# Kernel tuning notes

Measured on AMD Instinct MI355X. Metric: run time of the kernel, lower is better.

The kernel has to match this reference:

```python
import jax, jax.numpy as jnp
import numpy as np

S, T, B, V, E, H = 64, 48, 32, 32000, 512, 512


def setup_inputs() -> dict:
    key = jax.random.key(0)
    ks = jax.random.split(key, 24)
    def n(k, shape, s=0.05):
        return jax.random.normal(k, shape, dtype=jnp.float32) * s
    return {
        "src": jax.random.randint(ks[0], (S, B), 0, V),
        "trg": jax.random.randint(ks[1], (T, B), 0, V),
        "enc_emb": n(ks[2], (V, E)),
        "enc_Wih0": n(ks[3], (3 * H, E)),
        "enc_Whh0": n(ks[4], (3 * H, H)),
        "enc_bih0": n(ks[5], (3 * H,)),
        "enc_bhh0": n(ks[6], (3 * H,)),
        "enc_Wih1": n(ks[7], (3 * H, H)),
        "enc_Whh1": n(ks[8], (3 * H, H)),
        "enc_bih1": n(ks[9], (3 * H,)),
        "enc_bhh1": n(ks[10], (3 * H,)),
        "dec_emb": n(ks[11], (V, E)),
        "dec_Wih0": n(ks[12], (3 * H, E)),
        "dec_Whh0": n(ks[13], (3 * H, H)),
        "dec_bih0": n(ks[14], (3 * H,)),
        "dec_bhh0": n(ks[15], (3 * H,)),
        "dec_Wih1": n(ks[16], (3 * H, H)),
        "dec_Whh1": n(ks[17], (3 * H, H)),
        "dec_bih1": n(ks[18], (3 * H,)),
        "dec_bhh1": n(ks[19], (3 * H,)),
        "out_W": n(ks[20], (V, H)),
        "out_b": n(ks[21], (V,)),
    }


def gru_layer(xs, h0, Wih, Whh, bih, bhh):
    """PyTorch-convention GRU over a (T, B, D) sequence. Returns (ys, h_T)."""
    def step(h, x):
        gi = x @ Wih.T + bih          # (B, 3H)
        gh = h @ Whh.T + bhh          # (B, 3H)
        ir, iz, inn = jnp.split(gi, 3, axis=-1)
        hr, hz, hn = jnp.split(gh, 3, axis=-1)
        r = jax.nn.sigmoid(ir + hr)
        z = jax.nn.sigmoid(iz + hz)
        cand = jnp.tanh(inn + r * hn)
        h_new = (1.0 - z) * cand + z * h
        return h_new, h_new
    hT, ys = jax.lax.scan(step, h0, xs)
    return ys, hT


def reference(src, trg, enc_emb, enc_Wih0, enc_Whh0, enc_bih0, enc_bhh0,
              enc_Wih1, enc_Whh1, enc_bih1, enc_bhh1,
              dec_emb, dec_Wih0, dec_Whh0, dec_bih0, dec_bhh0,
              dec_Wih1, dec_Whh1, dec_bih1, dec_bhh1, out_W, out_b):
    b = src.shape[1]
    h = enc_Whh0.shape[1]
    h0 = jnp.zeros((b, h), dtype=enc_emb.dtype)
    # Encoder: 2-layer unidirectional GRU (dropout=0, eval mode)
    x = enc_emb[src]                                   # (S, B, E)
    y0, h0_f = gru_layer(x, h0, enc_Wih0, enc_Whh0, enc_bih0, enc_bhh0)
    _, h1_f = gru_layer(y0, h0, enc_Wih1, enc_Whh1, enc_bih1, enc_bhh1)
    # decoder_hidden = encoder_hidden[-2:] -> (layer0 final, layer1 final)
    # Decoder with teacher_forcing_ratio = 1.0: inputs are trg[:-1]
    d = dec_emb[trg[:-1]]                              # (T-1, B, E)
    d0, _ = gru_layer(d, h0_f, dec_Wih0, dec_Whh0, dec_bih0, dec_bhh0)
    d1, _ = gru_layer(d0, h1_f, dec_Wih1, dec_Whh1, dec_bih1, dec_bhh1)
    logits = d1 @ out_W.T + out_b                      # (T-1, B, V)
    return logits
```

## Files before the change

### kernel.cpp

```cpp
#include <hip/hip_runtime.h>
#include <hip/hip_bf16.h>

typedef __bf16 bf16x8 __attribute__((ext_vector_type(8)));
typedef float  f32x4  __attribute__((ext_vector_type(4)));

__device__ __forceinline__ void store_bf8(__bf16* dst, float4 a, float4 b) {
  bf16x8 v;
  v[0] = (__bf16)a.x; v[1] = (__bf16)a.y; v[2] = (__bf16)a.z; v[3] = (__bf16)a.w;
  v[4] = (__bf16)b.x; v[5] = (__bf16)b.y; v[6] = (__bf16)b.z; v[7] = (__bf16)b.w;
  *(bf16x8*)dst = v;
}

__device__ __forceinline__ bf16x8 load_coh16(const __bf16* p) {
  union { unsigned long long u[2]; bf16x8 v; } r;
  r.u[0] = __hip_atomic_load((const unsigned long long*)p,     __ATOMIC_RELAXED, __HIP_MEMORY_SCOPE_AGENT);
  r.u[1] = __hip_atomic_load((const unsigned long long*)p + 1, __ATOMIC_RELAXED, __HIP_MEMORY_SCOPE_AGENT);
  return r.v;
}

__device__ __forceinline__ void store_coh_bf16(__bf16* p, float v) {
  __bf16 b = (__bf16)v;
  unsigned short u;
  __builtin_memcpy(&u, &b, 2);
  __hip_atomic_store((unsigned short*)p, u, __ATOMIC_RELAXED, __HIP_MEMORY_SCOPE_AGENT);
}

__device__ __forceinline__ void wait_flags(const unsigned* f, unsigned tgt) {
  const unsigned* p = f + (threadIdx.x & 31) * 32;
  for (;;) {
    const unsigned v = __hip_atomic_load(p, __ATOMIC_RELAXED, __HIP_MEMORY_SCOPE_AGENT);
    if (__all((int)(v >= tgt))) break;
    __builtin_amdgcn_s_sleep(1);
  }
}

__global__ __launch_bounds__(256) void cvt_f32_bf16(
    const float* __restrict__ s, __bf16* __restrict__ d, long n8)
{
  long i = (long)blockIdx.x * 256 + threadIdx.x;
  if (i >= n8) return;
  const float4* sp = (const float4*)s + i * 2;
  store_bf8(d + i * 8, sp[0], sp[1]);
}

__global__ __launch_bounds__(64) void gather_cvt(
    const float* __restrict__ emb, const int* __restrict__ idx, __bf16* __restrict__ dst)
{
  const int r = blockIdx.x;
  const long row = idx[r];
  const float4* sp = (const float4*)(emb + row * 512) + threadIdx.x * 2;
  store_bf8(dst + (long)r * 512 + threadIdx.x * 8, sp[0], sp[1]);
}

__global__ __launch_bounds__(256) void gemm_bt(
    const __bf16* __restrict__ A, const __bf16* __restrict__ B,
    const float* __restrict__ bias, float* __restrict__ C, int M, int N)
{
  const int wave = threadIdx.x >> 6;
  const int lane = threadIdx.x & 63;
  const int l16 = lane & 15;
  const int quad = lane >> 4;

  const int m0 = blockIdx.x * 128 + wave * 32;
  const int n0 = blockIdx.y * 128;

  int r0 = m0 + l16;       if (r0 >= M) r0 = M - 1;
  int r1 = m0 + 16 + l16;  if (r1 >= M) r1 = M - 1;
  const __bf16* __restrict__ A0 = A + (long)r0 * 512 + quad * 8;
  const __bf16* __restrict__ A1 = A + (long)r1 * 512 + quad * 8;

  const __bf16* bp[8];
#pragma unroll
  for (int i = 0; i < 8; ++i)
    bp[i] = B + (long)(n0 + i * 16 + l16) * 512 + quad * 8;

  f32x4 acc[2][8];
#pragma unroll
  for (int mi = 0; mi < 2; ++mi)
#pragma unroll
    for (int i = 0; i < 8; ++i) acc[mi][i] = (f32x4){0.f, 0.f, 0.f, 0.f};

#pragma unroll
  for (int ks = 0; ks < 16; ++ks) {
    bf16x8 a0 = *(const bf16x8*)(A0 + ks * 32);
    bf16x8 a1 = *(const bf16x8*)(A1 + ks * 32);
#pragma unroll
    for (int i = 0; i < 8; ++i) {
      bf16x8 b = *(const bf16x8*)(bp[i] + ks * 32);
      acc[0][i] = __builtin_amdgcn_mfma_f32_16x16x32_bf16(a0, b, acc[0][i], 0, 0, 0);
      acc[1][i] = __builtin_amdgcn_mfma_f32_16x16x32_bf16(a1, b, acc[1][i], 0, 0, 0);
    }
  }

#pragma unroll
  for (int mi = 0; mi < 2; ++mi) {
    const int crow = m0 + mi * 16 + quad * 4;
#pragma unroll
    for (int i = 0; i < 8; ++i) {
      const int n = n0 + i * 16 + l16;
      const float bv = bias ? bias[n] : 0.0f;
#pragma unroll
      for (int r = 0; r < 4; ++r) {
        const int row = crow + r;
        if (row < M) C[(long)row * N + n] = acc[mi][i][r] + bv;
      }
    }
  }
}

__global__ __launch_bounds__(128) void gru2_pipe(
    const float* __restrict__ GI,
    const float* __restrict__ Whh0, const float* __restrict__ bhh0,
    const float* __restrict__ Wih1, const float* __restrict__ bih1,
    const float* __restrict__ Whh1, const float* __restrict__ bhh1,
    __bf16* __restrict__ Y0, __bf16* __restrict__ Y1,
    const __bf16* __restrict__ h0i, const __bf16* __restrict__ h1i,
    float* __restrict__ hf0, float* __restrict__ hf1,
    unsigned* __restrict__ flags0, unsigned* __restrict__ flags1, int T)
{
  __shared__ __align__(16) __bf16 wh[48 * 520];
  __shared__ __align__(16) __bf16 wi[48 * 520];

  const int tid = threadIdx.x;
  const int L   = blockIdx.x >> 5;
  const int c   = blockIdx.x & 31;
  const int w   = tid >> 6;
  const int lane = tid & 63;
  const int l16 = lane & 15;
  const int quad = lane >> 4;

  const float* __restrict__ Whh = L ? Whh1 : Whh0;
  const float* __restrict__ bhh = L ? bhh1 : bhh0;
  __bf16* __restrict__ Yown = L ? Y1 : Y0;
  const __bf16* __restrict__ hini = L ? h1i : h0i;
  float* __restrict__ hf = L ? hf1 : hf0;
  unsigned* __restrict__ fOwn = L ? flags1 : flags0;

  for (int ch = tid; ch < 48 * 64; ch += 128) {
    const int lr = ch >> 6, kc = ch & 63;
    const int g = lr >> 4, j = lr & 15;
    const float4* sp = (const float4*)(Whh + (long)(g * 512 + c * 16 + j) * 512) + kc * 2;
    store_bf8(&wh[lr * 520 + kc * 8], sp[0], sp[1]);
  }
  if (L) {
    for (int ch = tid; ch < 48 * 64; ch += 128) {
      const int lr = ch >> 6, kc = ch & 63;
      const int g = lr >> 4, j = lr & 15;
      const float4* sp = (const float4*)(Wih1 + (long)(g * 512 + c * 16 + j) * 512) + kc * 2;
      store_bf8(&wi[lr * 520 + kc * 8], sp[0], sp[1]);
    }
  }

  float bR = bhh[0 * 512 + c * 16 + l16];
  float bZ = bhh[1 * 512 + c * 16 + l16];
  float bH = bhh[2 * 512 + c * 16 + l16];
  float bN = 0.f;
  if (L) {
    bR += bih1[0 * 512 + c * 16 + l16];
    bZ += bih1[1 * 512 + c * 16 + l16];
    bN  = bih1[2 * 512 + c * 16 + l16];
  }
  __syncthreads();

  const int b0  = w * 16 + quad * 4;
  const int col = c * 16 + l16;

  float hprev[4];
#pragma unroll
  for (int r = 0; r < 4; ++r) hprev[r] = hf[(b0 + r) * 512 + col];

  for (int t = 0; t < T; ++t) {
    float giR[4] = {0, 0, 0, 0}, giZ[4] = {0, 0, 0, 0}, giN[4] = {0, 0, 0, 0};
    if (!L) {
      const float* GIt = GI + (long)t * 49152;
#pragma unroll
      for (int r = 0; r < 4; ++r) {
        const float* gp = GIt + (b0 + r) * 1536 + col;
        giR[r] = gp[0];
        giZ[r] = gp[512];
        giN[r] = gp[1024];
      }
    }

    if (L) {
      wait_flags(flags0, (unsigned)(t + 1));
      if (t) wait_flags(flags1, (unsigned)t);
    } else if (t) {
      wait_flags(flags0, (unsigned)t);
    }

    const __bf16* hsrc = t ? (Yown + (long)t * 16384) : hini;
    const __bf16* hA = hsrc + (w * 16 + l16) * 512 + quad * 8;
    bf16x8 ha[16], xa[16];
#pragma unroll
    for (int ks = 0; ks < 16; ++ks) ha[ks] = load_coh16(hA + ks * 32);
    if (L) {
      const __bf16* xA = Y0 + (long)(t + 1) * 16384 + (w * 16 + l16) * 512 + quad * 8;
#pragma unroll
      for (int ks = 0; ks < 16; ++ks) xa[ks] = load_coh16(xA + ks * 32);
    }

    f32x4 accR = {bR, bR, bR, bR};
    f32x4 accZ = {bZ, bZ, bZ, bZ};
    f32x4 accH = {bH, bH, bH, bH};
    f32x4 accN = {bN, bN, bN, bN};

#pragma unroll
    for (int ks = 0; ks < 16; ++ks) {
      const int o = ks * 32 + quad * 8;
      accR = __builtin_amdgcn_mfma_f32_16x16x32_bf16(ha[ks], *(const bf16x8*)&wh[(     l16) * 520 + o], accR, 0, 0, 0);
      accZ = __builtin_amdgcn_mfma_f32_16x16x32_bf16(ha[ks], *(const bf16x8*)&wh[(16 + l16) * 520 + o], accZ, 0, 0, 0);
      accH = __builtin_amdgcn_mfma_f32_16x16x32_bf16(ha[ks], *(const bf16x8*)&wh[(32 + l16) * 520 + o], accH, 0, 0, 0);
    }
    if (L) {
#pragma unroll
      for (int ks = 0; ks < 16; ++ks) {
        const int o = ks * 32 + quad * 8;
        accR = __builtin_amdgcn_mfma_f32_16x16x32_bf16(xa[ks], *(const bf16x8*)&wi[(     l16) * 520 + o], accR, 0, 0, 0);
        accZ = __builtin_amdgcn_mfma_f32_16x16x32_bf16(xa[ks], *(const bf16x8*)&wi[(16 + l16) * 520 + o], accZ, 0, 0, 0);
        accN = __builtin_amdgcn_mfma_f32_16x16x32_bf16(xa[ks], *(const bf16x8*)&wi[(32 + l16) * 520 + o], accN, 0, 0, 0);
      }
    }

    __bf16* yout = Yown + (long)(t + 1) * 16384;
#pragma unroll
    for (int r = 0; r < 4; ++r) {
      float rs = accR[r], zs = accZ[r], hn = accH[r], nn = accN[r];
      if (!L) { rs += giR[r]; zs += giZ[r]; nn = giN[r]; }
      const float rg = 1.0f / (1.0f + expf(-rs));
      const float zg = 1.0f / (1.0f + expf(-zs));
      const float cand = tanhf(nn + rg * hn);
      const float hnew = (1.0f - zg) * cand + zg * hprev[r];
      hprev[r] = hnew;
      store_coh_bf16(yout + (b0 + r) * 512 + col, hnew);
    }

    asm volatile("s_waitcnt vmcnt(0)" ::: "memory");
    __syncthreads();
    if (tid == 0)
      __hip_atomic_store(fOwn + c * 32, (unsigned)(t + 1),
                         __ATOMIC_RELAXED, __HIP_MEMORY_SCOPE_AGENT);
  }

#pragma unroll
  for (int r = 0; r < 4; ++r) hf[(b0 + r) * 512 + col] = hprev[r];
}

extern "C" void kernel_launch(void* const* d_in, const int* in_sizes, int n_in,
                              void* d_out, int out_size, void* d_ws, size_t ws_size,
                              hipStream_t stream)
{
  const int* src = (const int*)d_in[0];
  const int* trg = (const int*)d_in[1];
  const float* enc_emb  = (const float*)d_in[2];
  const float* enc_Wih0 = (const float*)d_in[3];
  const float* enc_Whh0 = (const float*)d_in[4];
  const float* enc_bih0 = (const float*)d_in[5];
  const float* enc_bhh0 = (const float*)d_in[6];
  const float* enc_Wih1 = (const float*)d_in[7];
  const float* enc_Whh1 = (const float*)d_in[8];
  const float* enc_bih1 = (const float*)d_in[9];
  const float* enc_bhh1 = (const float*)d_in[10];
  const float* dec_emb  = (const float*)d_in[11];
  const float* dec_Wih0 = (const float*)d_in[12];
  const float* dec_Whh0 = (const float*)d_in[13];
  const float* dec_bih0 = (const float*)d_in[14];
  const float* dec_bhh0 = (const float*)d_in[15];
  const float* dec_Wih1 = (const float*)d_in[16];
  const float* dec_Whh1 = (const float*)d_in[17];
  const float* dec_bih1 = (const float*)d_in[18];
  const float* dec_bhh1 = (const float*)d_in[19];
  const float* out_W    = (const float*)d_in[20];
  const float* out_b    = (const float*)d_in[21];

  char* ws = (char*)d_ws;
  float*  GI    = (float*)(ws + 0);
  __bf16* Xenc  = (__bf16*)(ws + 12582912);
  __bf16* Xdec  = (__bf16*)(ws + 14680064);
  __bf16* Y0e   = (__bf16*)(ws + 16220160);
  __bf16* Y1e   = (__bf16*)(ws + 18350080);
  __bf16* Y0d   = (__bf16*)(ws + 20480000);
  __bf16* Y1d   = (__bf16*)(ws + 22052864);
  __bf16* Wb0   = (__bf16*)(ws + 23625728);
  __bf16* Wb2   = (__bf16*)(ws + 25198592);
  __bf16* outWb = (__bf16*)(ws + 26771456);
  float*  hf0   = (float*)(ws + 59539456);
  float*  hf1   = (float*)(ws + 59604992);
  __bf16* zb    = (__bf16*)(ws + 59670528);
  unsigned* flags = (unsigned*)(ws + 59703296);

  hipMemsetAsync(hf0, 0, 131072, stream);
  hipMemsetAsync(zb, 0, 32768, stream);
  hipMemsetAsync(flags, 0, 16384, stream);

  gather_cvt<<<2048, 64, 0, stream>>>(enc_emb, src, Xenc);
  gather_cvt<<<1504, 64, 0, stream>>>(dec_emb, trg, Xdec);
  cvt_f32_bf16<<<384, 256, 0, stream>>>(enc_Wih0, Wb0, 98304);
  cvt_f32_bf16<<<384, 256, 0, stream>>>(dec_Wih0, Wb2, 98304);
  cvt_f32_bf16<<<8000, 256, 0, stream>>>(out_W, outWb, 2048000);

  gemm_bt<<<dim3(16, 12), 256, 0, stream>>>(Xenc, Wb0, enc_bih0, GI, 2048, 1536);
  gru2_pipe<<<64, 128, 0, stream>>>(GI, enc_Whh0, enc_bhh0,
                                    enc_Wih1, enc_bih1, enc_Whh1, enc_bhh1,
                                    Y0e, Y1e, zb, zb, hf0, hf1,
                                    flags + 0, flags + 1024, 64);
  gemm_bt<<<dim3(12, 12), 256, 0, stream>>>(Xdec, Wb2, dec_bih0, GI, 1504, 1536);
  gru2_pipe<<<64, 128, 0, stream>>>(GI, dec_Whh0, dec_bhh0,
                                    dec_Wih1, dec_bih1, dec_Whh1, dec_bhh1,
                                    Y0d, Y1d, Y0e + 64 * 16384, Y1e + 64 * 16384, hf0, hf1,
                                    flags + 2048, flags + 3072, 47);

  gemm_bt<<<dim3(12, 250), 256, 0, stream>>>(Y1d + 16384, outWb, out_b,
                                             (float*)d_out, 1504, 32000);
}
```

Measured before the change: 1.431 ms.

## Overlap layer-1 input projection before hidden wait, batch h stores via LDS

In the pipelined two-layer GRU kernel, layer 1 now waits only on layer 0's flag, loads the input activations and runs the input-side MFMAs before it waits on its own recurrent flag. This takes that work off the critical path between timesteps. Hidden-state outputs are staged in LDS and written as 16-byte coherent stores (sc0 sc1 inline asm) instead of scattered 2-byte atomic stores. Sigmoid and tanh use fast intrinsics. The extra __syncthreads and the fast-math activations add some cost and reduce accuracy slightly.

New measurement: 1.299 ms. 9.2% less time.

```diff
diff --git a/kernel.cpp b/kernel.cpp
--- a/kernel.cpp
+++ b/kernel.cpp
@@ -18,11 +18,9 @@
   return r.v;
 }
 
-__device__ __forceinline__ void store_coh_bf16(__bf16* p, float v) {
-  __bf16 b = (__bf16)v;
-  unsigned short u;
-  __builtin_memcpy(&u, &b, 2);
-  __hip_atomic_store((unsigned short*)p, u, __ATOMIC_RELAXED, __HIP_MEMORY_SCOPE_AGENT);
+__device__ __forceinline__ void store_coh16B(__bf16* p, bf16x8 v) {
+  asm volatile("global_store_dwordx4 %0, %1, off sc0 sc1"
+               :: "v"(p), "v"(v) : "memory");
 }
 
 __device__ __forceinline__ void wait_flags(const unsigned* f, unsigned tgt) {
@@ -120,6 +118,7 @@
 {
   __shared__ __align__(16) __bf16 wh[48 * 520];
   __shared__ __align__(16) __bf16 wi[48 * 520];
+  __shared__ __align__(16) __bf16 hlds[32][16];
 
   const int tid = threadIdx.x;
   const int L   = blockIdx.x >> 5;
@@ -182,37 +181,17 @@
       }
     }
 
-    if (L) {
-      wait_flags(flags0, (unsigned)(t + 1));
-      if (t) wait_flags(flags1, (unsigned)t);
-    } else if (t) {
-      wait_flags(flags0, (unsigned)t);
-    }
-
-    const __bf16* hsrc = t ? (Yown + (long)t * 16384) : hini;
-    const __bf16* hA = hsrc + (w * 16 + l16) * 512 + quad * 8;
-    bf16x8 ha[16], xa[16];
-#pragma unroll
-    for (int ks = 0; ks < 16; ++ks) ha[ks] = load_coh16(hA + ks * 32);
-    if (L) {
-      const __bf16* xA = Y0 + (long)(t + 1) * 16384 + (w * 16 + l16) * 512 + quad * 8;
-#pragma unroll
-      for (int ks = 0; ks < 16; ++ks) xa[ks] = load_coh16(xA + ks * 32);
-    }
-
     f32x4 accR = {bR, bR, bR, bR};
     f32x4 accZ = {bZ, bZ, bZ, bZ};
     f32x4 accH = {bH, bH, bH, bH};
     f32x4 accN = {bN, bN, bN, bN};
 
-#pragma unroll
-    for (int ks = 0; ks < 16; ++ks) {
-      const int o = ks * 32 + quad * 8;
-      accR = __builtin_amdgcn_mfma_f32_16x16x32_bf16(ha[ks], *(const bf16x8*)&wh[(     l16) * 520 + o], accR, 0, 0, 0);
-      accZ = __builtin_amdgcn_mfma_f32_16x16x32_bf16(ha[ks], *(const bf16x8*)&wh[(16 + l16) * 520 + o], accZ, 0, 0, 0);
-      accH = __builtin_amdgcn_mfma_f32_16x16x32_bf16(ha[ks], *(const bf16x8*)&wh[(32 + l16) * 520 + o], accH, 0, 0, 0);
-    }
     if (L) {
+      wait_flags(flags0, (unsigned)(t + 1));
+      const __bf16* xA = Y0 + (long)(t + 1) * 16384 + (w * 16 + l16) * 512 + quad * 8;
+      bf16x8 xa[16];
+#pragma unroll
+      for (int ks = 0; ks < 16; ++ks) xa[ks] = load_coh16(xA + ks * 32);
 #pragma unroll
       for (int ks = 0; ks < 16; ++ks) {
         const int o = ks * 32 + quad * 8;
@@ -220,21 +199,45 @@
         accZ = __builtin_amdgcn_mfma_f32_16x16x32_bf16(xa[ks], *(const bf16x8*)&wi[(16 + l16) * 520 + o], accZ, 0, 0, 0);
         accN = __builtin_amdgcn_mfma_f32_16x16x32_bf16(xa[ks], *(const bf16x8*)&wi[(32 + l16) * 520 + o], accN, 0, 0, 0);
       }
-    }
-
-    __bf16* yout = Yown + (long)(t + 1) * 16384;
+      if (t) wait_flags(flags1, (unsigned)t);
+    } else if (t) {
+      wait_flags(flags0, (unsigned)t);
+    }
+
+    const __bf16* hsrc = t ? (Yown + (long)t * 16384) : hini;
+    const __bf16* hA = hsrc + (w * 16 + l16) * 512 + quad * 8;
+    bf16x8 ha[16];
+#pragma unroll
+    for (int ks = 0; ks < 16; ++ks) ha[ks] = load_coh16(hA + ks * 32);
+#pragma unroll
+    for (int ks = 0; ks < 16; ++ks) {
+      const int o = ks * 32 + quad * 8;
+      accR = __builtin_amdgcn_mfma_f32_16x16x32_bf16(ha[ks], *(const bf16x8*)&wh[(     l16) * 520 + o], accR, 0, 0, 0);
+      accZ = __builtin_amdgcn_mfma_f32_16x16x32_bf16(ha[ks], *(const bf16x8*)&wh[(16 + l16) * 520 + o], accZ, 0, 0, 0);
+      accH = __builtin_amdgcn_mfma_f32_16x16x32_bf16(ha[ks], *(const bf16x8*)&wh[(32 + l16) * 520 + o], accH, 0, 0, 0);
+    }
+
 #pragma unroll
     for (int r = 0; r < 4; ++r) {
       float rs = accR[r], zs = accZ[r], hn = accH[r], nn = accN[r];
       if (!L) { rs += giR[r]; zs += giZ[r]; nn = giN[r]; }
-      const float rg = 1.0f / (1.0f + expf(-rs));
-      const float zg = 1.0f / (1.0f + expf(-zs));
-      const float cand = tanhf(nn + rg * hn);
+      const float rg = __fdividef(1.0f, 1.0f + __expf(-rs));
+      const float zg = __fdividef(1.0f, 1.0f + __expf(-zs));
+      const float a2 = nn + rg * hn;
+      const float e2 = __expf(2.0f * a2);
+      const float cand = 1.0f - __fdividef(2.0f, e2 + 1.0f);
       const float hnew = (1.0f - zg) * cand + zg * hprev[r];
       hprev[r] = hnew;
-      store_coh_bf16(yout + (b0 + r) * 512 + col, hnew);
-    }
-
+      hlds[b0 + r][l16] = (__bf16)hnew;
+    }
+    __syncthreads();
+
+    __bf16* yout = Yown + (long)(t + 1) * 16384;
+    if (tid < 64) {
+      const int row = tid >> 1, half = tid & 1;
+      bf16x8 hv = *(const bf16x8*)&hlds[row][half * 8];
+      store_coh16B(yout + (long)row * 512 + c * 16 + half * 8, hv);
+    }
     asm volatile("s_waitcnt vmcnt(0)" ::: "memory");
     __syncthreads();
     if (tid == 0)
```
